# Optimization experiments

Hardware: AMD Instinct MI355X
Metric: run time of the kernel (lower is better)

## Reference

```python
import jax, jax.numpy as jnp
import numpy as np

N_BUCKET, EPB, K, TAU = 4, 4, 2, 1.0
C, H = 512, 1024
E = N_BUCKET * EPB
B, T = 2, 1024

def _l2norm(v):
    # matches F.normalize(dim=-1): v / max(||v||, 1e-12)
    return v / jnp.maximum(jnp.linalg.norm(v, axis=-1, keepdims=True), 1e-12)

def setup_inputs() -> dict:
    key = jax.random.key(0)
    ks = jax.random.split(key, 8)
    s = 1.0 / np.sqrt(C).astype(np.float32)
    sh = 1.0 / np.sqrt(H).astype(np.float32)
    return {
        "x": jax.random.normal(ks[0], (B, T, C), jnp.float32),
        "op_id": jax.random.randint(ks[1], (B, T), 0, N_BUCKET),
        "expert_key": jax.random.normal(ks[2], (N_BUCKET, EPB, C), jnp.float32) * s,
        "sW1": jax.random.normal(ks[3], (C, H), jnp.float32) * s,
        "sb1": jnp.zeros((H,), jnp.float32),
        "sW2": jax.random.normal(ks[4], (H, C), jnp.float32) * sh,
        "sb2": jnp.zeros((C,), jnp.float32),
        "eW1": jax.random.normal(ks[5], (E, C, H), jnp.float32) * s,
        "eb1": jnp.zeros((E, H), jnp.float32),
        "eW2": jax.random.normal(ks[6], (E, H, C), jnp.float32) * sh,
        "eb2": jnp.zeros((E, C), jnp.float32),
        "gate_logit": jnp.float32(-2.0),
    }

def reference(x, op_id, expert_key, sW1, sb1, sW2, sb2, eW1, eb1, eW2, eb2, gate_logit):
    Bb, Tt, Cc = x.shape
    # --- HierKVRouter ---
    bucket = jnp.clip(op_id, 0, N_BUCKET - 1)                 # (B,T)
    h_n = _l2norm(x)                                          # (B,T,C)
    keys = _l2norm(expert_key)                                # (nb,epb,C)
    keys_bt = keys[bucket]                                    # (B,T,epb,C) gather
    score = jnp.einsum('btc,btec->bte', h_n, keys_bt) / max(TAU, 1e-6)
    probs_local = jax.nn.softmax(score, axis=-1)              # (B,T,epb)
    topv, local = jax.lax.top_k(probs_local, K)               # (B,T,K)
    w = topv / (jnp.sum(topv, axis=-1, keepdims=True) + 1e-9) # combine weights
    gid = bucket[..., None] * EPB + local                     # (B,T,K) global ids
    # --- dispatch / expert MLP / combine ---
    flat_in = jnp.broadcast_to(x[:, :, None, :], (Bb, Tt, K, Cc)).reshape(-1, Cc)
    flat_gid = gid.reshape(-1)                                # (B*T*K,)
    flat_w = w.reshape(-1)                                    # (B*T*K,)
    out = jnp.zeros_like(flat_in)
    for e in range(E):  # fixed small expert count; masked dense = exact math of torch boolean-mask loop
        mask = (flat_gid == e)[:, None]
        h1 = jax.nn.relu(flat_in @ eW1[e] + eb1[e])
        oe = h1 @ eW2[e] + eb2[e]
        out = out + jnp.where(mask, oe * flat_w[:, None], 0.0)
    moe_out = out.reshape(Bb, Tt, K, Cc).sum(axis=2)          # (B,T,C)
    # --- shared dense FFN + gated combine ---
    dense = jax.nn.relu(x @ sW1 + sb1) @ sW2 + sb2
    y = dense + jax.nn.sigmoid(gate_logit) * moe_out
    return y
```

## Files before the change

kernel.cpp:

```cpp
#include <hip/hip_runtime.h>
#include <hip/hip_bf16.h>
#include <math.h>

#define C_DIM 512
#define H_DIM 1024
#define NTOK  2048
#define NSLOT 4096
#define NROWS 6144
#define MAXT128 64
#define MAXT64  112

typedef __attribute__((ext_vector_type(8))) short short8;
typedef __attribute__((ext_vector_type(4))) float floatx4;
typedef __attribute__((address_space(3))) void as3_void;
typedef const __attribute__((address_space(1))) void as1_cvoid;

__device__ __forceinline__ void gload_lds16(const void* g, void* l){
  __builtin_amdgcn_global_load_lds((as1_cvoid*)g, (as3_void*)l, 16, 0, 0);
}

__device__ __forceinline__ unsigned short f2b(float f){
  unsigned int u = __float_as_uint(f);
  unsigned int r = (u + 0x7FFFu + ((u >> 16) & 1u)) >> 16;
  return (unsigned short)r;
}

__device__ __forceinline__ void transpose_tile(const float* __restrict__ in,
                                               unsigned short* __restrict__ out,
                                               int K, int N, int n0, int k0,
                                               int tid, float* tile){
  int tx = tid & 15, ty = tid >> 4;
  #pragma unroll
  for (int i = 0; i < 8; i++){
    int k = ty + 16 * i;
    float4 v = *reinterpret_cast<const float4*>(in + (size_t)(k0 + k) * N + n0 + tx * 4);
    tile[(4*tx + 0) * 129 + k] = v.x;
    tile[(4*tx + 1) * 129 + k] = v.y;
    tile[(4*tx + 2) * 129 + k] = v.z;
    tile[(4*tx + 3) * 129 + k] = v.w;
  }
  __syncthreads();
  int wt = tid & 31, wr = tid >> 5;
  #pragma unroll
  for (int i = 0; i < 8; i++){
    int n = wr + 8 * i;
    float4 v = *reinterpret_cast<const float4*>(&tile[n * 129 + 4 * wt]);
    ushort4 o;
    o.x = f2b(v.x); o.y = f2b(v.y); o.z = f2b(v.z); o.w = f2b(v.w);
    *reinterpret_cast<ushort4*>(out + (size_t)(n0 + n) * K + k0 + 4 * wt) = o;
  }
}

__global__ __launch_bounds__(256) void k_prep(const float* __restrict__ x,
                                              const int* __restrict__ op_id,
                                              const float* __restrict__ ekey,
                                              const float* __restrict__ sW1,
                                              const float* __restrict__ eW1,
                                              unsigned short* __restrict__ Xb,
                                              unsigned short* __restrict__ sW1t,
                                              unsigned short* __restrict__ eW1t,
                                              int* __restrict__ gids,
                                              float* __restrict__ wv){
  __shared__ __align__(16) float tile[64 * 129];
  const int bid = blockIdx.x;
  const int tid = threadIdx.x;
  const int g = bid / 25, r = bid % 25;

  if (r < 8){
    int u = g * 8 + r;
    int t = u * 4 + (tid >> 6);
    int lane = tid & 63;
    const float* xr = x + (size_t)t * C_DIM;
    {
      const float4* xr4 = reinterpret_cast<const float4*>(xr);
      float4 a = xr4[lane * 2], b = xr4[lane * 2 + 1];
      short8 o;
      o[0] = (short)f2b(a.x); o[1] = (short)f2b(a.y); o[2] = (short)f2b(a.z); o[3] = (short)f2b(a.w);
      o[4] = (short)f2b(b.x); o[5] = (short)f2b(b.y); o[6] = (short)f2b(b.z); o[7] = (short)f2b(b.w);
      *reinterpret_cast<short8*>(Xb + (size_t)t * C_DIM + lane * 8) = o;
    }
    float xs[8];
    float xn2 = 0.f;
    #pragma unroll
    for (int i = 0; i < 8; i++){ float v = xr[lane + 64*i]; xs[i] = v; xn2 += v*v; }
    #pragma unroll
    for (int o = 32; o; o >>= 1) xn2 += __shfl_xor(xn2, o, 64);
    int bucket = min(max(op_id[t], 0), 3);
    float xn = fmaxf(sqrtf(xn2), 1e-12f);
    float pr[4];
    #pragma unroll
    for (int e = 0; e < 4; e++){
      const float* kr = ekey + ((size_t)bucket * 4 + e) * C_DIM;
      float dot = 0.f, kn2 = 0.f;
      #pragma unroll
      for (int i = 0; i < 8; i++){ float kv = kr[lane + 64*i]; dot += xs[i]*kv; kn2 += kv*kv; }
      #pragma unroll
      for (int o = 32; o; o >>= 1){ dot += __shfl_xor(dot, o, 64); kn2 += __shfl_xor(kn2, o, 64); }
      float kn = fmaxf(sqrtf(kn2), 1e-12f);
      pr[e] = dot / (xn * kn);
    }
    float mx = fmaxf(fmaxf(pr[0], pr[1]), fmaxf(pr[2], pr[3]));
    float Z = 0.f;
    #pragma unroll
    for (int e = 0; e < 4; e++){ pr[e] = expf(pr[e] - mx); Z += pr[e]; }
    #pragma unroll
    for (int e = 0; e < 4; e++) pr[e] /= Z;
    int i0 = 0;
    #pragma unroll
    for (int e = 1; e < 4; e++) if (pr[e] > pr[i0]) i0 = e;
    int i1 = (i0 == 0) ? 1 : 0;
    #pragma unroll
    for (int e = 0; e < 4; e++) if (e != i0 && e != i1 && pr[e] > pr[i1]) i1 = e;
    float v0 = pr[i0], v1 = pr[i1];
    float wsum = v0 + v1 + 1e-9f;
    if (lane == 0){
      gids[2*t]   = bucket * 4 + i0;
      gids[2*t+1] = bucket * 4 + i1;
      wv[2*t]   = v0 / wsum;
      wv[2*t+1] = v1 / wsum;
    }
    return;
  }

  int wi = g * 17 + (r - 8);
  int mat = wi >> 6, tl = wi & 63;
  const float* in  = (mat < 16) ? eW1 + (size_t)mat * C_DIM * H_DIM : sW1;
  unsigned short* out = (mat < 16) ? eW1t + (size_t)mat * C_DIM * H_DIM : sW1t;
  transpose_tile(in, out, C_DIM, H_DIM, (tl & 15) * 64, (tl >> 4) * 128, tid, tile);
}

__global__ __launch_bounds__(256) void k_sort(const int* __restrict__ gids,
                                              const float* __restrict__ wv,
                                              const float* __restrict__ gate,
                                              int* __restrict__ inv,
                                              int* __restrict__ rowTok,
                                              float* __restrict__ rowW,
                                              int* __restrict__ tiles128,
                                              int* __restrict__ tiles64){
  __shared__ int hist[256][16];
  __shared__ int off[17];
  int tid = threadIdx.x;
  float sig = 1.f / (1.f + expf(-gate[0]));
  int h[16], g_[16];
  #pragma unroll
  for (int e = 0; e < 16; e++) h[e] = 0;
  int base = tid * 16;
  #pragma unroll
  for (int s = 0; s < 16; s++){ g_[s] = gids[base + s]; h[g_[s]]++; }
  #pragma unroll
  for (int e = 0; e < 16; e++) hist[tid][e] = h[e];
  __syncthreads();
  for (int d = 1; d < 256; d <<= 1){
    int v[16];
    if (tid >= d){
      #pragma unroll
      for (int e = 0; e < 16; e++) v[e] = hist[tid - d][e];
    }
    __syncthreads();
    if (tid >= d){
      #pragma unroll
      for (int e = 0; e < 16; e++) hist[tid][e] += v[e];
    }
    __syncthreads();
  }
  if (tid == 0){
    off[0] = 0;
    for (int e = 0; e < 16; e++) off[e+1] = off[e] + hist[255][e];
  }
  __syncthreads();
  int c[16];
  #pragma unroll
  for (int e = 0; e < 16; e++) c[e] = off[e] + hist[tid][e] - h[e];
  #pragma unroll
  for (int s = 0; s < 16; s++){
    int slot = base + s;
    int g = g_[s];
    int pos = c[g]++;
    inv[slot] = pos;
    rowTok[NTOK + pos] = slot >> 1;
    rowW[NTOK + pos] = sig * wv[slot];
  }
  for (int rr = tid; rr < NTOK; rr += 256){ rowTok[rr] = rr; rowW[rr] = 1.0f; }
  __syncthreads();
  if (tid == 0){
    int nt = 0;
    for (int r0 = 0; r0 < NTOK; r0 += 128){
      tiles128[nt*3] = r0; tiles128[nt*3+1] = 128; tiles128[nt*3+2] = 16; nt++;
    }
    for (int e = 0; e < 16; e++){
      int cc = off[e+1] - off[e];
      for (int r0 = 0; r0 < cc; r0 += 128){
        tiles128[nt*3] = NTOK + off[e] + r0;
        tiles128[nt*3+1] = min(128, cc - r0);
        tiles128[nt*3+2] = e;
        nt++;
      }
    }
    for (int i = nt; i < MAXT128; i++){ tiles128[i*3] = 0; tiles128[i*3+1] = 0; tiles128[i*3+2] = 0; }
    nt = 0;
    for (int r0 = 0; r0 < NTOK; r0 += 64){
      tiles64[nt*3] = r0; tiles64[nt*3+1] = 64; tiles64[nt*3+2] = 16; nt++;
    }
    for (int e = 0; e < 16; e++){
      int cc = off[e+1] - off[e];
      for (int r0 = 0; r0 < cc; r0 += 64){
        tiles64[nt*3] = NTOK + off[e] + r0;
        tiles64[nt*3+1] = min(64, cc - r0);
        tiles64[nt*3+2] = e;
        nt++;
      }
    }
    for (int i = nt; i < MAXT64; i++){ tiles64[i*3] = 0; tiles64[i*3+1] = 0; tiles64[i*3+2] = 0; }
  }
}

__global__ __launch_bounds__(256) void k_g1w2(const unsigned short* __restrict__ A,
                                              const unsigned short* __restrict__ BtE,
                                              const unsigned short* __restrict__ BtS,
                                              const float* __restrict__ biasE,
                                              const float* __restrict__ biasS,
                                              const int* __restrict__ rowTok,
                                              const int* __restrict__ tiles,
                                              unsigned short* __restrict__ outB,
                                              const float* __restrict__ sW2,
                                              const float* __restrict__ eW2,
                                              unsigned short* __restrict__ sW2t,
                                              unsigned short* __restrict__ eW2t){
  __shared__ __align__(16) char smem[65536];
  const int bx = blockIdx.x;
  const int tid = threadIdx.x;
  const int g = bx / 25, r = bx % 25;

  if (r >= 8){
    int wi = g * 17 + (r - 8);
    int mat = wi >> 6, tl = wi & 63;
    const float* in  = (mat < 16) ? eW2 + (size_t)mat * H_DIM * C_DIM : sW2;
    unsigned short* out = (mat < 16) ? eW2t + (size_t)mat * H_DIM * C_DIM : sW2t;
    transpose_tile(in, out, H_DIM, C_DIM, (tl & 7) * 64, (tl >> 3) * 128, tid, (float*)smem);
    return;
  }

  constexpr int KDIM = C_DIM, NDIM = H_DIM;
  const int gi = g * 8 + r;
  const int tileId = gi >> 3;
  const int rows = tiles[tileId*3+1];
  if (rows == 0) return;
  const int row0 = tiles[tileId*3];
  const int eid  = tiles[tileId*3+2];
  const unsigned short* Bt = (eid < 16) ? (BtE + (size_t)eid * NDIM * KDIM) : BtS;
  const float* bias = (eid < 16) ? (biasE + eid * NDIM) : biasS;
  const int n0 = (gi & 7) * 128;

  unsigned short (*As)[128*64] = (unsigned short(*)[128*64])smem;
  unsigned short (*Bs)[128*64] = (unsigned short(*)[128*64])(smem + 32768);

  const int lane = tid & 63;
  const int wid = tid >> 6;
  const int wm = wid >> 1, wn = wid & 1;
  const int l15 = lane & 15, lhi = lane >> 4;

  int aRow[4], aOff[4], bRow[4], bOff[4];
  #pragma unroll
  for (int j = 0; j < 4; j++){
    int c = j * 256 + tid;
    int i = c >> 3, op = c & 7;
    int o = op ^ (i & 7);
    int ie = min(i, rows - 1);
    aRow[j] = rowTok[row0 + ie];
    aOff[j] = o * 8;
    bRow[j] = n0 + i;
    bOff[j] = o * 8;
  }

  auto STAGE = [&](int buf, int kt){
    #pragma unroll
    for (int j = 0; j < 4; j++)
      gload_lds16(A + (size_t)aRow[j] * KDIM + kt * 64 + aOff[j],
                  (char*)&As[buf][0] + (j * 256 + tid) * 16);
    #pragma unroll
    for (int j = 0; j < 4; j++)
      gload_lds16(Bt + (size_t)bRow[j] * KDIM + kt * 64 + bOff[j],
                  (char*)&Bs[buf][0] + (j * 256 + tid) * 16);
  };

  floatx4 acc[4][4] = {};
  constexpr int NT = KDIM / 64;

  STAGE(0, 0);
  for (int kt = 0; kt < NT; ++kt){
    const int cur = kt & 1;
    if (kt + 1 < NT){
      STAGE(cur ^ 1, kt + 1);
      asm volatile("s_waitcnt vmcnt(8)" ::: "memory");
    } else {
      asm volatile("s_waitcnt vmcnt(0)" ::: "memory");
    }
    __builtin_amdgcn_s_barrier();
    asm volatile("" ::: "memory");
    #pragma unroll
    for (int kk = 0; kk < 2; ++kk){
      short8 a[4], b[4];
      #pragma unroll
      for (int m = 0; m < 4; m++){
        int rr = wm * 64 + m * 16 + l15;
        a[m] = *reinterpret_cast<const short8*>(
            (char*)&As[cur][0] + rr * 128 + ((kk * 64 + lhi * 16) ^ ((rr & 7) << 4)));
      }
      #pragma unroll
      for (int n = 0; n < 4; n++){
        int rr = wn * 64 + n * 16 + l15;
        b[n] = *reinterpret_cast<const short8*>(
            (char*)&Bs[cur][0] + rr * 128 + ((kk * 64 + lhi * 16) ^ ((rr & 7) << 4)));
      }
      #pragma unroll
      for (int m = 0; m < 4; m++)
        #pragma unroll
        for (int n = 0; n < 4; n++)
          acc[m][n] = __builtin_amdgcn_mfma_f32_16x16x32_bf16(a[m], b[n], acc[m][n], 0, 0, 0);
    }
    asm volatile("" ::: "memory");
    __builtin_amdgcn_s_barrier();
  }

  #pragma unroll
  for (int m = 0; m < 4; m++){
    #pragma unroll
    for (int n = 0; n < 4; n++){
      int gcol = n0 + wn * 64 + n * 16 + l15;
      float bv = bias[gcol];
      #pragma unroll
      for (int q = 0; q < 4; q++){
        int ri = wm * 64 + m * 16 + lhi * 4 + q;
        if (ri < rows){
          float v = fmaxf(acc[m][n][q] + bv, 0.f);
          outB[(size_t)(row0 + ri) * NDIM + gcol] = f2b(v);
        }
      }
    }
  }
}

template<int BMT, int KDIM, int NDIM>
__global__ __launch_bounds__(256) void k_gemm2(const unsigned short* __restrict__ A,
                                               const unsigned short* __restrict__ BtE,
                                               const unsigned short* __restrict__ BtS,
                                               const float* __restrict__ biasE,
                                               const float* __restrict__ biasS,
                                               const float* __restrict__ rowW,
                                               const int* __restrict__ tiles,
                                               float* __restrict__ outF){
  const int tileId = blockIdx.x;
  const int rows = tiles[tileId*3+1];
  if (rows == 0) return;
  const int row0 = tiles[tileId*3];
  const int eid  = tiles[tileId*3+2];
  const unsigned short* Bt = (eid < 16) ? (BtE + (size_t)eid * NDIM * KDIM) : BtS;
  const float* bias = (eid < 16) ? (biasE + eid * NDIM) : biasS;
  const int n0 = blockIdx.y * 128;

  constexpr int MREP = BMT / 32;
  constexpr int AISS = BMT * 8 / 256;

  __shared__ __align__(16) unsigned short As[2][BMT * 64];
  __shared__ __align__(16) unsigned short Bs[2][128 * 64];

  const int tid = threadIdx.x;
  const int lane = tid & 63;
  const int wid = tid >> 6;
  const int wm = wid >> 1, wn = wid & 1;
  const int l15 = lane & 15, lhi = lane >> 4;

  int aRow[AISS], aOff[AISS];
  #pragma unroll
  for (int j = 0; j < AISS; j++){
    int c = j * 256 + tid;
    int i = c >> 3, op = c & 7;
    int o = op ^ (i & 7);
    int ie = min(i, rows - 1);
    aRow[j] = row0 + ie;
    aOff[j] = o * 8;
  }
  int bRow[4], bOff[4];
  #pragma unroll
  for (int j = 0; j < 4; j++){
    int c = j * 256 + tid;
    int i = c >> 3, op = c & 7;
    int o = op ^ (i & 7);
    bRow[j] = n0 + i;
    bOff[j] = o * 8;
  }

  auto STAGE = [&](int buf, int kt){
    #pragma unroll
    for (int j = 0; j < AISS; j++)
      gload_lds16(A + (size_t)aRow[j] * KDIM + kt * 64 + aOff[j],
                  (char*)&As[buf][0] + (j * 256 + tid) * 16);
    #pragma unroll
    for (int j = 0; j < 4; j++)
      gload_lds16(Bt + (size_t)bRow[j] * KDIM + kt * 64 + bOff[j],
                  (char*)&Bs[buf][0] + (j * 256 + tid) * 16);
  };

  floatx4 acc[MREP][4] = {};
  constexpr int NT = KDIM / 64;

  STAGE(0, 0);
  for (int kt = 0; kt < NT; ++kt){
    const int cur = kt & 1;
    if (kt + 1 < NT){
      STAGE(cur ^ 1, kt + 1);
      asm volatile("s_waitcnt vmcnt(6)" ::: "memory");
    } else {
      asm volatile("s_waitcnt vmcnt(0)" ::: "memory");
    }
    __builtin_amdgcn_s_barrier();
    asm volatile("" ::: "memory");
    #pragma unroll
    for (int kk = 0; kk < 2; ++kk){
      short8 a[MREP], b[4];
      #pragma unroll
      for (int m = 0; m < MREP; m++){
        int rr = wm * (BMT/2) + m * 16 + l15;
        a[m] = *reinterpret_cast<const short8*>(
            (char*)&As[cur][0] + rr * 128 + ((kk * 64 + lhi * 16) ^ ((rr & 7) << 4)));
      }
      #pragma unroll
      for (int n = 0; n < 4; n++){
        int rr = wn * 64 + n * 16 + l15;
        b[n] = *reinterpret_cast<const short8*>(
            (char*)&Bs[cur][0] + rr * 128 + ((kk * 64 + lhi * 16) ^ ((rr & 7) << 4)));
      }
      #pragma unroll
      for (int m = 0; m < MREP; m++)
        #pragma unroll
        for (int n = 0; n < 4; n++)
          acc[m][n] = __builtin_amdgcn_mfma_f32_16x16x32_bf16(a[m], b[n], acc[m][n], 0, 0, 0);
    }
    asm volatile("" ::: "memory");
    __builtin_amdgcn_s_barrier();
  }

  #pragma unroll
  for (int m = 0; m < MREP; m++){
    #pragma unroll
    for (int n = 0; n < 4; n++){
      int gcol = n0 + wn * 64 + n * 16 + l15;
      float bv = bias[gcol];
      #pragma unroll
      for (int q = 0; q < 4; q++){
        int ri = wm * (BMT/2) + m * 16 + lhi * 4 + q;
        if (ri < rows){
          float v = (acc[m][n][q] + bv) * rowW[row0 + ri];
          outF[(size_t)(row0 + ri) * NDIM + gcol] = v;
        }
      }
    }
  }
}

__global__ __launch_bounds__(256) void k_combine(const float* __restrict__ O,
                                                 const int* __restrict__ inv,
                                                 float* __restrict__ y){
  int q = blockIdx.x * 256 + threadIdx.x;
  int t = q >> 7, c4 = q & 127;
  const float4* Of = reinterpret_cast<const float4*>(O);
  float4 d  = Of[(size_t)t * 128 + c4];
  int p0 = inv[2*t], p1 = inv[2*t+1];
  float4 o0 = Of[(size_t)(NTOK + p0) * 128 + c4];
  float4 o1 = Of[(size_t)(NTOK + p1) * 128 + c4];
  float4 r;
  r.x = d.x + o0.x + o1.x;
  r.y = d.y + o0.y + o1.y;
  r.z = d.z + o0.z + o1.z;
  r.w = d.w + o0.w + o1.w;
  reinterpret_cast<float4*>(y)[q] = r;
}

extern "C" void kernel_launch(void* const* d_in, const int* in_sizes, int n_in,
                              void* d_out, int out_size, void* d_ws, size_t ws_size,
                              hipStream_t stream){
  const float* x    = (const float*)d_in[0];
  const int*   opid = (const int*)d_in[1];
  const float* ekey = (const float*)d_in[2];
  const float* sW1  = (const float*)d_in[3];
  const float* sb1  = (const float*)d_in[4];
  const float* sW2  = (const float*)d_in[5];
  const float* sb2  = (const float*)d_in[6];
  const float* eW1  = (const float*)d_in[7];
  const float* eb1  = (const float*)d_in[8];
  const float* eW2  = (const float*)d_in[9];
  const float* eb2  = (const float*)d_in[10];
  const float* gate = (const float*)d_in[11];
  float* y = (float*)d_out;

  char* ws = (char*)d_ws;
  size_t off = 0;
  auto alloc = [&](size_t bytes) -> char* {
    char* p = ws + off; off += (bytes + 255) & ~(size_t)255; return p;
  };
  unsigned short* Xb   = (unsigned short*)alloc((size_t)NTOK * C_DIM * 2);
  unsigned short* sW1t = (unsigned short*)alloc((size_t)H_DIM * C_DIM * 2);
  unsigned short* sW2t = (unsigned short*)alloc((size_t)C_DIM * H_DIM * 2);
  unsigned short* eW1t = (unsigned short*)alloc((size_t)16 * H_DIM * C_DIM * 2);
  unsigned short* eW2t = (unsigned short*)alloc((size_t)16 * C_DIM * H_DIM * 2);
  unsigned short* H1   = (unsigned short*)alloc((size_t)NROWS * H_DIM * 2);
  float* O      = (float*)alloc((size_t)NROWS * C_DIM * 4);
  float* wv     = (float*)alloc((size_t)NSLOT * 4);
  int*   gids   = (int*)alloc((size_t)NSLOT * 4);
  int*   inv    = (int*)alloc((size_t)NSLOT * 4);
  int*   rowTok = (int*)alloc((size_t)NROWS * 4);
  float* rowW   = (float*)alloc((size_t)NROWS * 4);
  int*   tiles128 = (int*)alloc((size_t)MAXT128 * 3 * 4);
  int*   tiles64  = (int*)alloc((size_t)MAXT64 * 3 * 4);

  k_prep<<<1600, 256, 0, stream>>>(x, opid, ekey, sW1, eW1, Xb, sW1t, eW1t, gids, wv);
  k_sort<<<1, 256, 0, stream>>>(gids, wv, gate, inv, rowTok, rowW, tiles128, tiles64);
  k_g1w2<<<1600, 256, 0, stream>>>(Xb, eW1t, sW1t, eb1, sb1, rowTok, tiles128, H1,
                                   sW2, eW2, sW2t, eW2t);
  k_gemm2<64, H_DIM, C_DIM><<<dim3(MAXT64, C_DIM/128), 256, 0, stream>>>(
      H1, eW2t, sW2t, eb2, sb2, rowW, tiles64, O);
  k_combine<<<1024, 256, 0, stream>>>(O, inv, y);
}
```

Measured before the change: 90.19 us.

## Use 256-row tiles with 512-thread GEMMs and move W2 transposes into prep

All weight transposes, including W2, now run in the prep kernel, so the first GEMM no longer shares its launch with the W2 transpose blocks. Both GEMMs switch to 256-row M tiles with 512 threads (8 waves) and a single shared tile list, which cuts per-tile B reloads and the number of padded tail tiles. GEMM2's N tile shrinks to 64 to keep the block count up. The trade-offs are fewer blocks overall, more padding waste in the per-expert tail tiles, and a larger LDS footprint that can lower occupancy.

After: 87.22 us. 3.3% less time.

```diff
diff --git a/kernel.cpp b/kernel.cpp
--- a/kernel.cpp
+++ b/kernel.cpp
@@ -7,8 +7,7 @@
 #define NTOK  2048
 #define NSLOT 4096
 #define NROWS 6144
-#define MAXT128 64
-#define MAXT64  112
+#define MAXT  40
 
 typedef __attribute__((ext_vector_type(8))) short short8;
 typedef __attribute__((ext_vector_type(4))) float floatx4;
@@ -56,77 +55,86 @@
                                               const float* __restrict__ ekey,
                                               const float* __restrict__ sW1,
                                               const float* __restrict__ eW1,
+                                              const float* __restrict__ sW2,
+                                              const float* __restrict__ eW2,
                                               unsigned short* __restrict__ Xb,
                                               unsigned short* __restrict__ sW1t,
                                               unsigned short* __restrict__ eW1t,
+                                              unsigned short* __restrict__ sW2t,
+                                              unsigned short* __restrict__ eW2t,
                                               int* __restrict__ gids,
                                               float* __restrict__ wv){
   __shared__ __align__(16) float tile[64 * 129];
   const int bid = blockIdx.x;
   const int tid = threadIdx.x;
-  const int g = bid / 25, r = bid % 25;
-
-  if (r < 8){
-    int u = g * 8 + r;
-    int t = u * 4 + (tid >> 6);
-    int lane = tid & 63;
-    const float* xr = x + (size_t)t * C_DIM;
-    {
-      const float4* xr4 = reinterpret_cast<const float4*>(xr);
-      float4 a = xr4[lane * 2], b = xr4[lane * 2 + 1];
-      short8 o;
-      o[0] = (short)f2b(a.x); o[1] = (short)f2b(a.y); o[2] = (short)f2b(a.z); o[3] = (short)f2b(a.w);
-      o[4] = (short)f2b(b.x); o[5] = (short)f2b(b.y); o[6] = (short)f2b(b.z); o[7] = (short)f2b(b.w);
-      *reinterpret_cast<short8*>(Xb + (size_t)t * C_DIM + lane * 8) = o;
-    }
-    float xs[8];
-    float xn2 = 0.f;
-    #pragma unroll
-    for (int i = 0; i < 8; i++){ float v = xr[lane + 64*i]; xs[i] = v; xn2 += v*v; }
-    #pragma unroll
-    for (int o = 32; o; o >>= 1) xn2 += __shfl_xor(xn2, o, 64);
-    int bucket = min(max(op_id[t], 0), 3);
-    float xn = fmaxf(sqrtf(xn2), 1e-12f);
-    float pr[4];
-    #pragma unroll
-    for (int e = 0; e < 4; e++){
-      const float* kr = ekey + ((size_t)bucket * 4 + e) * C_DIM;
-      float dot = 0.f, kn2 = 0.f;
-      #pragma unroll
-      for (int i = 0; i < 8; i++){ float kv = kr[lane + 64*i]; dot += xs[i]*kv; kn2 += kv*kv; }
-      #pragma unroll
-      for (int o = 32; o; o >>= 1){ dot += __shfl_xor(dot, o, 64); kn2 += __shfl_xor(kn2, o, 64); }
-      float kn = fmaxf(sqrtf(kn2), 1e-12f);
-      pr[e] = dot / (xn * kn);
-    }
-    float mx = fmaxf(fmaxf(pr[0], pr[1]), fmaxf(pr[2], pr[3]));
-    float Z = 0.f;
-    #pragma unroll
-    for (int e = 0; e < 4; e++){ pr[e] = expf(pr[e] - mx); Z += pr[e]; }
-    #pragma unroll
-    for (int e = 0; e < 4; e++) pr[e] /= Z;
-    int i0 = 0;
-    #pragma unroll
-    for (int e = 1; e < 4; e++) if (pr[e] > pr[i0]) i0 = e;
-    int i1 = (i0 == 0) ? 1 : 0;
-    #pragma unroll
-    for (int e = 0; e < 4; e++) if (e != i0 && e != i1 && pr[e] > pr[i1]) i1 = e;
-    float v0 = pr[i0], v1 = pr[i1];
-    float wsum = v0 + v1 + 1e-9f;
-    if (lane == 0){
-      gids[2*t]   = bucket * 4 + i0;
-      gids[2*t+1] = bucket * 4 + i1;
-      wv[2*t]   = v0 / wsum;
-      wv[2*t+1] = v1 / wsum;
-    }
+
+  if (bid < 1088){
+    int mat = bid >> 6, tl = bid & 63;
+    const float* in  = (mat < 16) ? eW1 + (size_t)mat * C_DIM * H_DIM : sW1;
+    unsigned short* out = (mat < 16) ? eW1t + (size_t)mat * C_DIM * H_DIM : sW1t;
+    transpose_tile(in, out, C_DIM, H_DIM, (tl & 15) * 64, (tl >> 4) * 128, tid, tile);
     return;
   }
-
-  int wi = g * 17 + (r - 8);
-  int mat = wi >> 6, tl = wi & 63;
-  const float* in  = (mat < 16) ? eW1 + (size_t)mat * C_DIM * H_DIM : sW1;
-  unsigned short* out = (mat < 16) ? eW1t + (size_t)mat * C_DIM * H_DIM : sW1t;
-  transpose_tile(in, out, C_DIM, H_DIM, (tl & 15) * 64, (tl >> 4) * 128, tid, tile);
+  if (bid < 2176){
+    int wi = bid - 1088;
+    int mat = wi >> 6, tl = wi & 63;
+    const float* in  = (mat < 16) ? eW2 + (size_t)mat * H_DIM * C_DIM : sW2;
+    unsigned short* out = (mat < 16) ? eW2t + (size_t)mat * H_DIM * C_DIM : sW2t;
+    transpose_tile(in, out, H_DIM, C_DIM, (tl & 7) * 64, (tl >> 3) * 128, tid, tile);
+    return;
+  }
+  int u = bid - 2176;
+  int t = u * 4 + (tid >> 6);
+  int lane = tid & 63;
+  const float* xr = x + (size_t)t * C_DIM;
+  {
+    const float4* xr4 = reinterpret_cast<const float4*>(xr);
+    float4 a = xr4[lane * 2], b = xr4[lane * 2 + 1];
+    short8 o;
+    o[0] = (short)f2b(a.x); o[1] = (short)f2b(a.y); o[2] = (short)f2b(a.z); o[3] = (short)f2b(a.w);
+    o[4] = (short)f2b(b.x); o[5] = (short)f2b(b.y); o[6] = (short)f2b(b.z); o[7] = (short)f2b(b.w);
+    *reinterpret_cast<short8*>(Xb + (size_t)t * C_DIM + lane * 8) = o;
+  }
+  float xs[8];
+  float xn2 = 0.f;
+  #pragma unroll
+  for (int i = 0; i < 8; i++){ float v = xr[lane + 64*i]; xs[i] = v; xn2 += v*v; }
+  #pragma unroll
+  for (int o = 32; o; o >>= 1) xn2 += __shfl_xor(xn2, o, 64);
+  int bucket = min(max(op_id[t], 0), 3);
+  float xn = fmaxf(sqrtf(xn2), 1e-12f);
+  float pr[4];
+  #pragma unroll
+  for (int e = 0; e < 4; e++){
+    const float* kr = ekey + ((size_t)bucket * 4 + e) * C_DIM;
+    float dot = 0.f, kn2 = 0.f;
+    #pragma unroll
+    for (int i = 0; i < 8; i++){ float kv = kr[lane + 64*i]; dot += xs[i]*kv; kn2 += kv*kv; }
+    #pragma unroll
+    for (int o = 32; o; o >>= 1){ dot += __shfl_xor(dot, o, 64); kn2 += __shfl_xor(kn2, o, 64); }
+    float kn = fmaxf(sqrtf(kn2), 1e-12f);
+    pr[e] = dot / (xn * kn);
+  }
+  float mx = fmaxf(fmaxf(pr[0], pr[1]), fmaxf(pr[2], pr[3]));
+  float Z = 0.f;
+  #pragma unroll
+  for (int e = 0; e < 4; e++){ pr[e] = expf(pr[e] - mx); Z += pr[e]; }
+  #pragma unroll
+  for (int e = 0; e < 4; e++) pr[e] /= Z;
+  int i0 = 0;
+  #pragma unroll
+  for (int e = 1; e < 4; e++) if (pr[e] > pr[i0]) i0 = e;
+  int i1 = (i0 == 0) ? 1 : 0;
+  #pragma unroll
+  for (int e = 0; e < 4; e++) if (e != i0 && e != i1 && pr[e] > pr[i1]) i1 = e;
+  float v0 = pr[i0], v1 = pr[i1];
+  float wsum = v0 + v1 + 1e-9f;
+  if (lane == 0){
+    gids[2*t]   = bucket * 4 + i0;
+    gids[2*t+1] = bucket * 4 + i1;
+    wv[2*t]   = v0 / wsum;
+    wv[2*t+1] = v1 / wsum;
+  }
 }
 
 __global__ __launch_bounds__(256) void k_sort(const int* __restrict__ gids,
@@ -135,8 +143,7 @@
                                               int* __restrict__ inv,
                                               int* __restrict__ rowTok,
                                               float* __restrict__ rowW,
-                                              int* __restrict__ tiles128,
-                                              int* __restrict__ tiles64){
+                                              int* __restrict__ tiles){
   __shared__ int hist[256][16];
   __shared__ int off[17];
   int tid = threadIdx.x;
@@ -184,207 +191,64 @@
   __syncthreads();
   if (tid == 0){
     int nt = 0;
-    for (int r0 = 0; r0 < NTOK; r0 += 128){
-      tiles128[nt*3] = r0; tiles128[nt*3+1] = 128; tiles128[nt*3+2] = 16; nt++;
+    for (int r0 = 0; r0 < NTOK; r0 += 256){
+      tiles[nt*3] = r0; tiles[nt*3+1] = 256; tiles[nt*3+2] = 16; nt++;
     }
     for (int e = 0; e < 16; e++){
       int cc = off[e+1] - off[e];
-      for (int r0 = 0; r0 < cc; r0 += 128){
-        tiles128[nt*3] = NTOK + off[e] + r0;
-        tiles128[nt*3+1] = min(128, cc - r0);
-        tiles128[nt*3+2] = e;
+      for (int r0 = 0; r0 < cc; r0 += 256){
+        tiles[nt*3] = NTOK + off[e] + r0;
+        tiles[nt*3+1] = min(256, cc - r0);
+        tiles[nt*3+2] = e;
         nt++;
       }
     }
-    for (int i = nt; i < MAXT128; i++){ tiles128[i*3] = 0; tiles128[i*3+1] = 0; tiles128[i*3+2] = 0; }
-    nt = 0;
-    for (int r0 = 0; r0 < NTOK; r0 += 64){
-      tiles64[nt*3] = r0; tiles64[nt*3+1] = 64; tiles64[nt*3+2] = 16; nt++;
-    }
-    for (int e = 0; e < 16; e++){
-      int cc = off[e+1] - off[e];
-      for (int r0 = 0; r0 < cc; r0 += 64){
-        tiles64[nt*3] = NTOK + off[e] + r0;
-        tiles64[nt*3+1] = min(64, cc - r0);
-        tiles64[nt*3+2] = e;
-        nt++;
-      }
-    }
-    for (int i = nt; i < MAXT64; i++){ tiles64[i*3] = 0; tiles64[i*3+1] = 0; tiles64[i*3+2] = 0; }
-  }
-}
-
-__global__ __launch_bounds__(256) void k_g1w2(const unsigned short* __restrict__ A,
-                                              const unsigned short* __restrict__ BtE,
-                                              const unsigned short* __restrict__ BtS,
-                                              const float* __restrict__ biasE,
-                                              const float* __restrict__ biasS,
-                                              const int* __restrict__ rowTok,
-                                              const int* __restrict__ tiles,
-                                              unsigned short* __restrict__ outB,
-                                              const float* __restrict__ sW2,
-                                              const float* __restrict__ eW2,
-                                              unsigned short* __restrict__ sW2t,
-                                              unsigned short* __restrict__ eW2t){
-  __shared__ __align__(16) char smem[65536];
-  const int bx = blockIdx.x;
-  const int tid = threadIdx.x;
-  const int g = bx / 25, r = bx % 25;
-
-  if (r >= 8){
-    int wi = g * 17 + (r - 8);
-    int mat = wi >> 6, tl = wi & 63;
-    const float* in  = (mat < 16) ? eW2 + (size_t)mat * H_DIM * C_DIM : sW2;
-    unsigned short* out = (mat < 16) ? eW2t + (size_t)mat * H_DIM * C_DIM : sW2t;
-    transpose_tile(in, out, H_DIM, C_DIM, (tl & 7) * 64, (tl >> 3) * 128, tid, (float*)smem);
-    return;
-  }
-
+    for (int i = nt; i < MAXT; i++){ tiles[i*3] = 0; tiles[i*3+1] = 0; tiles[i*3+2] = 0; }
+  }
+}
+
+__global__ __launch_bounds__(512) void k_gemm1(const unsigned short* __restrict__ A,
+                                               const unsigned short* __restrict__ BtE,
+                                               const unsigned short* __restrict__ BtS,
+                                               const float* __restrict__ biasE,
+                                               const float* __restrict__ biasS,
+                                               const int* __restrict__ rowTok,
+                                               const int* __restrict__ tiles,
+                                               unsigned short* __restrict__ outB){
   constexpr int KDIM = C_DIM, NDIM = H_DIM;
-  const int gi = g * 8 + r;
-  const int tileId = gi >> 3;
+  const int tileId = blockIdx.x >> 3;
   const int rows = tiles[tileId*3+1];
   if (rows == 0) return;
   const int row0 = tiles[tileId*3];
   const int eid  = tiles[tileId*3+2];
   const unsigned short* Bt = (eid < 16) ? (BtE + (size_t)eid * NDIM * KDIM) : BtS;
   const float* bias = (eid < 16) ? (biasE + eid * NDIM) : biasS;
-  const int n0 = (gi & 7) * 128;
-
-  unsigned short (*As)[128*64] = (unsigned short(*)[128*64])smem;
-  unsigned short (*Bs)[128*64] = (unsigned short(*)[128*64])(smem + 32768);
-
+  const int n0 = (blockIdx.x & 7) * 128;
+
+  __shared__ __align__(16) unsigned short As[2][256 * 64];
+  __shared__ __align__(16) unsigned short Bs[2][128 * 64];
+
+  const int tid = threadIdx.x;
   const int lane = tid & 63;
   const int wid = tid >> 6;
-  const int wm = wid >> 1, wn = wid & 1;
+  const int wm = wid >> 2, wn = wid & 3;
   const int l15 = lane & 15, lhi = lane >> 4;
 
-  int aRow[4], aOff[4], bRow[4], bOff[4];
+  int aRow[4], aOff[4];
   #pragma unroll
   for (int j = 0; j < 4; j++){
-    int c = j * 256 + tid;
-    int i = c >> 3, op = c & 7;
+    int cc = j * 512 + tid;
+    int i = cc >> 3, op = cc & 7;
     int o = op ^ (i & 7);
     int ie = min(i, rows - 1);
     aRow[j] = rowTok[row0 + ie];
     aOff[j] = o * 8;
-    bRow[j] = n0 + i;
-    bOff[j] = o * 8;
-  }
-
-  auto STAGE = [&](int buf, int kt){
-    #pragma unroll
-    for (int j = 0; j < 4; j++)
-      gload_lds16(A + (size_t)aRow[j] * KDIM + kt * 64 + aOff[j],
-                  (char*)&As[buf][0] + (j * 256 + tid) * 16);
-    #pragma unroll
-    for (int j = 0; j < 4; j++)
-      gload_lds16(Bt + (size_t)bRow[j] * KDIM + kt * 64 + bOff[j],
-                  (char*)&Bs[buf][0] + (j * 256 + tid) * 16);
-  };
-
-  floatx4 acc[4][4] = {};
-  constexpr int NT = KDIM / 64;
-
-  STAGE(0, 0);
-  for (int kt = 0; kt < NT; ++kt){
-    const int cur = kt & 1;
-    if (kt + 1 < NT){
-      STAGE(cur ^ 1, kt + 1);
-      asm volatile("s_waitcnt vmcnt(8)" ::: "memory");
-    } else {
-      asm volatile("s_waitcnt vmcnt(0)" ::: "memory");
-    }
-    __builtin_amdgcn_s_barrier();
-    asm volatile("" ::: "memory");
-    #pragma unroll
-    for (int kk = 0; kk < 2; ++kk){
-      short8 a[4], b[4];
-      #pragma unroll
-      for (int m = 0; m < 4; m++){
-        int rr = wm * 64 + m * 16 + l15;
-        a[m] = *reinterpret_cast<const short8*>(
-            (char*)&As[cur][0] + rr * 128 + ((kk * 64 + lhi * 16) ^ ((rr & 7) << 4)));
-      }
-      #pragma unroll
-      for (int n = 0; n < 4; n++){
-        int rr = wn * 64 + n * 16 + l15;
-        b[n] = *reinterpret_cast<const short8*>(
-            (char*)&Bs[cur][0] + rr * 128 + ((kk * 64 + lhi * 16) ^ ((rr & 7) << 4)));
-      }
-      #pragma unroll
-      for (int m = 0; m < 4; m++)
-        #pragma unroll
-        for (int n = 0; n < 4; n++)
-          acc[m][n] = __builtin_amdgcn_mfma_f32_16x16x32_bf16(a[m], b[n], acc[m][n], 0, 0, 0);
-    }
-    asm volatile("" ::: "memory");
-    __builtin_amdgcn_s_barrier();
-  }
-
-  #pragma unroll
-  for (int m = 0; m < 4; m++){
-    #pragma unroll
-    for (int n = 0; n < 4; n++){
-      int gcol = n0 + wn * 64 + n * 16 + l15;
-      float bv = bias[gcol];
-      #pragma unroll
-      for (int q = 0; q < 4; q++){
-        int ri = wm * 64 + m * 16 + lhi * 4 + q;
-        if (ri < rows){
-          float v = fmaxf(acc[m][n][q] + bv, 0.f);
-          outB[(size_t)(row0 + ri) * NDIM + gcol] = f2b(v);
-        }
-      }
-    }
-  }
-}
-
-template<int BMT, int KDIM, int NDIM>
-__global__ __launch_bounds__(256) void k_gemm2(const unsigned short* __restrict__ A,
-                                               const unsigned short* __restrict__ BtE,
-                                               const unsigned short* __restrict__ BtS,
-                                               const float* __restrict__ biasE,
-                                               const float* __restrict__ biasS,
-                                               const float* __restrict__ rowW,
-                                               const int* __restrict__ tiles,
-                                               float* __restrict__ outF){
-  const int tileId = blockIdx.x;
-  const int rows = tiles[tileId*3+1];
-  if (rows == 0) return;
-  const int row0 = tiles[tileId*3];
-  const int eid  = tiles[tileId*3+2];
-  const unsigned short* Bt = (eid < 16) ? (BtE + (size_t)eid * NDIM * KDIM) : BtS;
-  const float* bias = (eid < 16) ? (biasE + eid * NDIM) : biasS;
-  const int n0 = blockIdx.y * 128;
-
-  constexpr int MREP = BMT / 32;
-  constexpr int AISS = BMT * 8 / 256;
-
-  __shared__ __align__(16) unsigned short As[2][BMT * 64];
-  __shared__ __align__(16) unsigned short Bs[2][128 * 64];
-
-  const int tid = threadIdx.x;
-  const int lane = tid & 63;
-  const int wid = tid >> 6;
-  const int wm = wid >> 1, wn = wid & 1;
-  const int l15 = lane & 15, lhi = lane >> 4;
-
-  int aRow[AISS], aOff[AISS];
-  #pragma unroll
-  for (int j = 0; j < AISS; j++){
-    int c = j * 256 + tid;
-    int i = c >> 3, op = c & 7;
-    int o = op ^ (i & 7);
-    int ie = min(i, rows - 1);
-    aRow[j] = row0 + ie;
-    aOff[j] = o * 8;
-  }
-  int bRow[4], bOff[4];
-  #pragma unroll
-  for (int j = 0; j < 4; j++){
-    int c = j * 256 + tid;
-    int i = c >> 3, op = c & 7;
+  }
+  int bRow[2], bOff[2];
+  #pragma unroll
+  for (int j = 0; j < 2; j++){
+    int cc = j * 512 + tid;
+    int i = cc >> 3, op = cc & 7;
     int o = op ^ (i & 7);
     bRow[j] = n0 + i;
     bOff[j] = o * 8;
@@ -392,16 +256,16 @@
 
   auto STAGE = [&](int buf, int kt){
     #pragma unroll
-    for (int j = 0; j < AISS; j++)
+    for (int j = 0; j < 4; j++)
       gload_lds16(A + (size_t)aRow[j] * KDIM + kt * 64 + aOff[j],
-                  (char*)&As[buf][0] + (j * 256 + tid) * 16);
-    #pragma unroll
-    for (int j = 0; j < 4; j++)
+                  (char*)&As[buf][0] + (j * 512 + tid) * 16);
+    #pragma unroll
+    for (int j = 0; j < 2; j++)
       gload_lds16(Bt + (size_t)bRow[j] * KDIM + kt * 64 + bOff[j],
-                  (char*)&Bs[buf][0] + (j * 256 + tid) * 16);
+                  (char*)&Bs[buf][0] + (j * 512 + tid) * 16);
   };
 
-  floatx4 acc[MREP][4] = {};
+  floatx4 acc[8][2] = {};
   constexpr int NT = KDIM / 64;
 
   STAGE(0, 0);
@@ -417,23 +281,23 @@
     asm volatile("" ::: "memory");
     #pragma unroll
     for (int kk = 0; kk < 2; ++kk){
-      short8 a[MREP], b[4];
-      #pragma unroll
-      for (int m = 0; m < MREP; m++){
-        int rr = wm * (BMT/2) + m * 16 + l15;
+      short8 a[8], b[2];
+      #pragma unroll
+      for (int m = 0; m < 8; m++){
+        int r = wm * 128 + m * 16 + l15;
         a[m] = *reinterpret_cast<const short8*>(
-            (char*)&As[cur][0] + rr * 128 + ((kk * 64 + lhi * 16) ^ ((rr & 7) << 4)));
-      }
-      #pragma unroll
-      for (int n = 0; n < 4; n++){
-        int rr = wn * 64 + n * 16 + l15;
+            (char*)&As[cur][0] + r * 128 + ((kk * 64 + lhi * 16) ^ ((r & 7) << 4)));
+      }
+      #pragma unroll
+      for (int n = 0; n < 2; n++){
+        int r = wn * 32 + n * 16 + l15;
         b[n] = *reinterpret_cast<const short8*>(
-            (char*)&Bs[cur][0] + rr * 128 + ((kk * 64 + lhi * 16) ^ ((rr & 7) << 4)));
-      }
-      #pragma unroll
-      for (int m = 0; m < MREP; m++)
+            (char*)&Bs[cur][0] + r * 128 + ((kk * 64 + lhi * 16) ^ ((r & 7) << 4)));
+      }
+      #pragma unroll
+      for (int m = 0; m < 8; m++)
         #pragma unroll
-        for (int n = 0; n < 4; n++)
+        for (int n = 0; n < 2; n++)
           acc[m][n] = __builtin_amdgcn_mfma_f32_16x16x32_bf16(a[m], b[n], acc[m][n], 0, 0, 0);
     }
     asm volatile("" ::: "memory");
@@ -441,14 +305,125 @@
   }
 
   #pragma unroll
-  for (int m = 0; m < MREP; m++){
-    #pragma unroll
-    for (int n = 0; n < 4; n++){
-      int gcol = n0 + wn * 64 + n * 16 + l15;
+  for (int m = 0; m < 8; m++){
+    #pragma unroll
+    for (int n = 0; n < 2; n++){
+      int gcol = n0 + wn * 32 + n * 16 + l15;
       float bv = bias[gcol];
       #pragma unroll
       for (int q = 0; q < 4; q++){
-        int ri = wm * (BMT/2) + m * 16 + lhi * 4 + q;
+        int ri = wm * 128 + m * 16 + lhi * 4 + q;
+        if (ri < rows){
+          float v = fmaxf(acc[m][n][q] + bv, 0.f);
+          outB[(size_t)(row0 + ri) * NDIM + gcol] = f2b(v);
+        }
+      }
+    }
+  }
+}
+
+__global__ __launch_bounds__(512) void k_gemm2(const unsigned short* __restrict__ A,
+                                               const unsigned short* __restrict__ BtE,
+                                               const unsigned short* __restrict__ BtS,
+                                               const float* __restrict__ biasE,
+                                               const float* __restrict__ biasS,
+                                               const float* __restrict__ rowW,
+                                               const int* __restrict__ tiles,
+                                               float* __restrict__ outF){
+  constexpr int KDIM = H_DIM, NDIM = C_DIM;
+  const int tileId = blockIdx.x >> 3;
+  const int rows = tiles[tileId*3+1];
+  if (rows == 0) return;
+  const int row0 = tiles[tileId*3];
+  const int eid  = tiles[tileId*3+2];
+  const unsigned short* Bt = (eid < 16) ? (BtE + (size_t)eid * NDIM * KDIM) : BtS;
+  const float* bias = (eid < 16) ? (biasE + eid * NDIM) : biasS;
+  const int n0 = (blockIdx.x & 7) * 64;
+
+  __shared__ __align__(16) unsigned short As[2][256 * 64];
+  __shared__ __align__(16) unsigned short Bs[2][64 * 64];
+
+  const int tid = threadIdx.x;
+  const int lane = tid & 63;
+  const int wid = tid >> 6;
+  const int wm = wid >> 1, wn = wid & 1;
+  const int l15 = lane & 15, lhi = lane >> 4;
+
+  int aRow[4], aOff[4];
+  #pragma unroll
+  for (int j = 0; j < 4; j++){
+    int cc = j * 512 + tid;
+    int i = cc >> 3, op = cc & 7;
+    int o = op ^ (i & 7);
+    int ie = min(i, rows - 1);
+    aRow[j] = row0 + ie;
+    aOff[j] = o * 8;
+  }
+  int bRow, bOff;
+  {
+    int i = tid >> 3, op = tid & 7;
+    int o = op ^ (i & 7);
+    bRow = n0 + i;
+    bOff = o * 8;
+  }
+
+  auto STAGE = [&](int buf, int kt){
+    #pragma unroll
+    for (int j = 0; j < 4; j++)
+      gload_lds16(A + (size_t)aRow[j] * KDIM + kt * 64 + aOff[j],
+                  (char*)&As[buf][0] + (j * 512 + tid) * 16);
+    gload_lds16(Bt + (size_t)bRow * KDIM + kt * 64 + bOff,
+                (char*)&Bs[buf][0] + tid * 16);
+  };
+
+  floatx4 acc[4][2] = {};
+  constexpr int NT = KDIM / 64;
+
+  STAGE(0, 0);
+  for (int kt = 0; kt < NT; ++kt){
+    const int cur = kt & 1;
+    if (kt + 1 < NT){
+      STAGE(cur ^ 1, kt + 1);
+      asm volatile("s_waitcnt vmcnt(5)" ::: "memory");
+    } else {
+      asm volatile("s_waitcnt vmcnt(0)" ::: "memory");
+    }
+    __builtin_amdgcn_s_barrier();
+    asm volatile("" ::: "memory");
+    #pragma unroll
+    for (int kk = 0; kk < 2; ++kk){
+      short8 a[4], b[2];
+      #pragma unroll
+      for (int m = 0; m < 4; m++){
+        int r = wm * 64 + m * 16 + l15;
+        a[m] = *reinterpret_cast<const short8*>(
+            (char*)&As[cur][0] + r * 128 + ((kk * 64 + lhi * 16) ^ ((r & 7) << 4)));
+      }
+      #pragma unroll
+      for (int n = 0; n < 2; n++){
+        int r = wn * 32 + n * 16 + l15;
+        b[n] = *reinterpret_cast<const short8*>(
+            (char*)&Bs[cur][0] + r * 128 + ((kk * 64 + lhi * 16) ^ ((r & 7) << 4)));
+      }
+      #pragma unroll
+      for (int m = 0; m < 4; m++)
+        #pragma unroll
+        for (int n = 0; n < 2; n++)
+          acc[m][n] = __builtin_amdgcn_mfma_f32_16x16x32_bf16(a[m], b[n], acc[m][n], 0, 0, 0);
+    }
+    asm volatile("" ::: "memory");
+    __builtin_amdgcn_s_barrier();
+  }
+
+  #pragma unroll
+  for (int m = 0; m < 4; m++){
+    #pragma unroll
+    for (int n = 0; n < 2; n++){
+      int gcol = n0 + wn * 32 + n * 16 + l15;
+      float bv = bias[gcol];
+      #pragma unroll
+      for (int q = 0; q < 4; q++){
+        int ri = wm * 64 + m * 16 + lhi * 4 + q;
         if (ri < rows){
           float v = (acc[m][n][q] + bv) * rowW[row0 + ri];
           outF[(size_t)(row0 + ri) * NDIM + gcol] = v;
@@ -510,14 +485,12 @@
   int*   inv    = (int*)alloc((size_t)NSLOT * 4);
   int*   rowTok = (int*)alloc((size_t)NROWS * 4);
   float* rowW   = (float*)alloc((size_t)NROWS * 4);
-  int*   tiles128 = (int*)alloc((size_t)MAXT128 * 3 * 4);
-  int*   tiles64  = (int*)alloc((size_t)MAXT64 * 3 * 4);
-
-  k_prep<<<1600, 256, 0, stream>>>(x, opid, ekey, sW1, eW1, Xb, sW1t, eW1t, gids, wv);
-  k_sort<<<1, 256, 0, stream>>>(gids, wv, gate, inv, rowTok, rowW, tiles128, tiles64);
-  k_g1w2<<<1600, 256, 0, stream>>>(Xb, eW1t, sW1t, eb1, sb1, rowTok, tiles128, H1,
-                                   sW2, eW2, sW2t, eW2t);
-  k_gemm2<64, H_DIM, C_DIM><<<dim3(MAXT64, C_DIM/128), 256, 0, stream>>>(
-      H1, eW2t, sW2t, eb2, sb2, rowW, tiles64, O);
+  int*   tiles  = (int*)alloc((size_t)MAXT * 3 * 4);
+
+  k_prep<<<2688, 256, 0, stream>>>(x, opid, ekey, sW1, eW1, sW2, eW2,
+                                   Xb, sW1t, eW1t, sW2t, eW2t, gids, wv);
+  k_sort<<<1, 256, 0, stream>>>(gids, wv, gate, inv, rowTok, rowW, tiles);
+  k_gemm1<<<MAXT * 8, 512, 0, stream>>>(Xb, eW1t, sW1t, eb1, sb1, rowTok, tiles, H1);
+  k_gemm2<<<MAXT * 8, 512, 0, stream>>>(H1, eW2t, sW2t, eb2, sb2, rowW, tiles, O);
   k_combine<<<1024, 256, 0, stream>>>(O, inv, y);
 }
```
